# Optimization experiments

Measured on AMD Instinct MI355X. Metric: run time of the kernel, lower is better.

The kernel has to match this reference:

```python
import jax, jax.numpy as jnp
import numpy as np
import math

N_HEADS = 4
IN_DIM = 1024
DIM_HEAD = IN_DIM // N_HEADS


def setup_inputs() -> dict:
    key = jax.random.key(0)
    ks = jax.random.split(key, 5)
    x = jax.random.normal(ks[0], (8, 2048, IN_DIM), dtype=jnp.float32)
    std = 0.02
    W_Q = jax.random.normal(ks[1], (N_HEADS, IN_DIM, DIM_HEAD), dtype=jnp.float32) * std
    W_K = jax.random.normal(ks[2], (N_HEADS, IN_DIM, DIM_HEAD), dtype=jnp.float32) * std
    W_V = jax.random.normal(ks[3], (N_HEADS, IN_DIM, DIM_HEAD), dtype=jnp.float32) * std
    W_O = jax.random.normal(ks[4], (N_HEADS, DIM_HEAD, IN_DIM), dtype=jnp.float32) * std
    b_Q = jnp.zeros((N_HEADS, DIM_HEAD), dtype=jnp.float32)
    b_K = jnp.zeros((N_HEADS, DIM_HEAD), dtype=jnp.float32)
    b_V = jnp.zeros((N_HEADS, DIM_HEAD), dtype=jnp.float32)
    b_O = jnp.zeros((IN_DIM,), dtype=jnp.float32)
    return {"normalized_resid_pre": x, "W_Q": W_Q, "b_Q": b_Q, "W_K": W_K,
            "b_K": b_K, "W_V": W_V, "b_V": b_V, "W_O": W_O, "b_O": b_O}


def reference(normalized_resid_pre, W_Q, b_Q, W_K, b_K, W_V, b_V, W_O, b_O):
    x = normalized_resid_pre  # [n, s, d_model]
    # projections: [n, s, h, dh]
    q = jnp.einsum('nsd,hde->nshe', x, W_Q) + b_Q
    k = jnp.einsum('nsd,hde->nshe', x, W_K) + b_K
    v = jnp.einsum('nsd,hde->nshe', x, W_V) + b_V
    scale = 1.0 / math.sqrt(DIM_HEAD)
    scores = jnp.einsum('nqhe,nkhe->nhqk', q, k) * scale  # [n, h, q, k]
    pattern = jax.nn.softmax(scores, axis=-1)
    z = jnp.einsum('nhqk,nkhe->nqhe', pattern, v)  # [n, q, h, dh]
    out = jnp.einsum('nqhe,hed->nqd', z, W_O) + b_O  # [n, q, d_model]
    return out
```

## Files before the change

kernel.cpp:

```cpp
#include <hip/hip_runtime.h>

typedef __attribute__((ext_vector_type(8))) short short8;
typedef __attribute__((ext_vector_type(4))) float floatx4;
typedef __attribute__((ext_vector_type(16))) float floatx16;
typedef __attribute__((ext_vector_type(4))) unsigned short ushort4v;
typedef __attribute__((ext_vector_type(2))) unsigned int uint2v;
typedef unsigned short u16;

__device__ __forceinline__ u16 f2bf(float f) {
  unsigned u = __float_as_uint(f);
  u += 0x7fffu + ((u >> 16) & 1u);
  return (u16)(u >> 16);
}

__device__ __forceinline__ void gl_lds16(const void* g, void* l) {
  __builtin_amdgcn_global_load_lds((const __attribute__((address_space(1))) void*)g,
                                   (__attribute__((address_space(3))) void*)l, 16, 0, 0);
}

__device__ __forceinline__ float bpermf(float v, int srclane) {
  return __int_as_float(__builtin_amdgcn_ds_bpermute(srclane << 2, __float_as_int(v)));
}

#define BARRIER() do { asm volatile("" ::: "memory"); __builtin_amdgcn_s_barrier(); asm volatile("" ::: "memory"); } while (0)


__global__ void k_cvt_x(const float* __restrict__ x, u16* __restrict__ o, long n) {
  long i = ((long)blockIdx.x * blockDim.x + threadIdx.x) * 8;
  long stride = (long)gridDim.x * blockDim.x * 8;
  for (; i < n; i += stride) {
    float4 a = *(const float4*)(x + i);
    float4 b = *(const float4*)(x + i + 4);
    ushort4v r0 = { f2bf(a.x), f2bf(a.y), f2bf(a.z), f2bf(a.w) };
    ushort4v r1 = { f2bf(b.x), f2bf(b.y), f2bf(b.z), f2bf(b.w) };
    *(ushort4v*)(o + i) = r0;
    *(ushort4v*)(o + i + 4) = r1;
  }
}

__global__ __launch_bounds__(256) void k_cvt_w(
    const float* __restrict__ WQ, const float* __restrict__ WK,
    const float* __restrict__ WV, const float* __restrict__ WO,
    u16* __restrict__ wqkv, u16* __restrict__ wo) {
  __shared__ float tile[64][65];
  const int bid = blockIdx.x;
  const float* src;
  u16* dst;
  int C, R, r0, c0;
  if (bid < 768) {
    int th = bid >> 6;
    int tid6 = bid & 63;
    int t = th >> 2, h = th & 3;
    src = ((t == 0) ? WQ : (t == 1) ? WK : WV) + h * 1024 * 256;
    dst = wqkv + (size_t)(t * 1024 + h * 256) * 1024;
    R = 1024; C = 256;
    r0 = (tid6 & 15) * 64;
    c0 = (tid6 >> 4) * 64;
  } else {
    int tid6 = bid - 768;
    src = WO; dst = wo;
    R = 1024; C = 1024;
    r0 = (tid6 & 15) * 64;
    c0 = (tid6 >> 4) * 64;
  }
  const int tx = threadIdx.x & 15, ty = threadIdx.x >> 4;
#pragma unroll
  for (int i = 0; i < 4; ++i) {
    int r = ty + 16 * i;
    float4 v = *(const float4*)(src + (long)(r0 + r) * C + c0 + tx * 4);
    tile[r][tx * 4 + 0] = v.x;
    tile[r][tx * 4 + 1] = v.y;
    tile[r][tx * 4 + 2] = v.z;
    tile[r][tx * 4 + 3] = v.w;
  }
  __syncthreads();
#pragma unroll
  for (int i = 0; i < 4; ++i) {
    int c = ty + 16 * i;
    ushort4v o = { f2bf(tile[tx * 4 + 0][c]), f2bf(tile[tx * 4 + 1][c]),
                   f2bf(tile[tx * 4 + 2][c]), f2bf(tile[tx * 4 + 3][c]) };
    *(ushort4v*)(dst + (long)(c0 + c) * R + r0 + tx * 4) = o;
  }
}

template<int EPI>
__global__ __launch_bounds__(512, 2) void k_gemm8(
    const u16* __restrict__ A, const u16* __restrict__ Bt,
    u16* __restrict__ Qo, u16* __restrict__ Ko, u16* __restrict__ Vt,
    const float* __restrict__ bQ, const float* __restrict__ bK, const float* __restrict__ bV,
    float* __restrict__ out, const float* __restrict__ bO, int gridNx) {
  extern __shared__ char lds[];
  const int tid = threadIdx.x, lane = tid & 63, w = tid >> 6;
  const int wm = w >> 2, wn = w & 3;
  const int cI = lane & 15, rI = lane >> 4;
  const int nwg = gridDim.x;
  const int bid = blockIdx.x;
  const int swz = (bid & 7) * (nwg >> 3) + (bid >> 3);
  const int by = swz / gridNx, bx = swz % gridNx;
  const long am0 = (long)by * 256, bn0 = (long)bx * 256;

  int so_ds[2], so_src[2];
#pragma unroll
  for (int jj = 0; jj < 2; ++jj) {
    int o = jj * 8192 + tid * 16;
    int row = o >> 7;
    so_ds[jj] = o;
    so_src[jj] = row * 1024 + ((((o >> 4) & 7) ^ (row & 7)) << 3);
  }
  const u16* gAlo = A + am0 * 1024;
  const u16* gAhi = gAlo + 128 * 1024;
  const u16* gBlo = Bt + bn0 * 1024;
  const u16* gBhi = gBlo + 128 * 1024;

#define STG(gp, kt, ldsbyte) do { \
    gl_lds16((gp) + (kt) * 64 + so_src[0], lds + (ldsbyte) + so_ds[0]); \
    gl_lds16((gp) + (kt) * 64 + so_src[1], lds + (ldsbyte) + so_ds[1]); \
  } while (0)

  floatx4 acc[8][4] = {};

  STG(gAlo, 0, 0);
  STG(gBlo, 0, 65536);
  STG(gAhi, 0, 16384);
  STG(gBhi, 0, 81920);
  STG(gAlo, 1, 32768);
  STG(gBlo, 1, 98304);
  asm volatile("s_waitcnt vmcnt(4)" ::: "memory");
  BARRIER();

#define PHASE(AB, BB, MH, NH, STAGE_STMT, VMSTMT) do { \
    short8 af[4][2], bf[2][2]; \
    _Pragma("unroll") \
    for (int mi2 = 0; mi2 < 4; ++mi2) { \
      int row = wm * 64 + mi2 * 16 + cI; \
      const char* rp = lds + (AB) + (MH) * 16384 + row * 128; \
      int sw = row & 7; \
      _Pragma("unroll") \
      for (int kk = 0; kk < 2; ++kk) \
        af[mi2][kk] = *(const short8*)(rp + (((kk * 4 + rI) ^ sw) << 4)); \
    } \
    _Pragma("unroll") \
    for (int ni2 = 0; ni2 < 2; ++ni2) { \
      int row = wn * 32 + ni2 * 16 + cI; \
      const char* rp = lds + (BB) + (NH) * 16384 + row * 128; \
      int sw = row & 7; \
      _Pragma("unroll") \
      for (int kk = 0; kk < 2; ++kk) \
        bf[ni2][kk] = *(const short8*)(rp + (((kk * 4 + rI) ^ sw) << 4)); \
    } \
    STAGE_STMT; \
    VMSTMT; \
    BARRIER(); \
    __builtin_amdgcn_s_setprio(1); \
    _Pragma("unroll") \
    for (int mi2 = 0; mi2 < 4; ++mi2) \
      _Pragma("unroll") \
      for (int ni2 = 0; ni2 < 2; ++ni2) \
        _Pragma("unroll") \
        for (int kk = 0; kk < 2; ++kk) \
          acc[(MH) * 4 + mi2][(NH) * 2 + ni2] = __builtin_amdgcn_mfma_f32_16x16x32_bf16( \
              af[mi2][kk], bf[ni2][kk], acc[(MH) * 4 + mi2][(NH) * 2 + ni2], 0, 0, 0); \
    __builtin_amdgcn_s_setprio(0); \
    BARRIER(); \
  } while (0)

  for (int it = 0; it < 8; ++it) {
    const int u = 2 * it;
    const bool s2 = (u + 2 < 16), s3 = (u + 3 < 16);
    PHASE(0, 65536, 0, 0, STG(gAhi, u + 1, 49152), );
    PHASE(0, 65536, 0, 1, STG(gBhi, u + 1, 114688), );
    PHASE(0, 65536, 1, 0, if (s2) STG(gAlo, u + 2, 0), );
    PHASE(0, 65536, 1, 1, if (s2) STG(gBlo, u + 2, 65536),
          if (s2) { asm volatile("s_waitcnt vmcnt(4)" ::: "memory"); }
          else    { asm volatile("s_waitcnt vmcnt(0)" ::: "memory"); });
    PHASE(32768, 98304, 0, 0, if (s2) STG(gAhi, u + 2, 16384), );
    PHASE(32768, 98304, 0, 1, if (s2) STG(gBhi, u + 2, 81920), );
    PHASE(32768, 98304, 1, 0, if (s3) STG(gAlo, u + 3, 32768), );
    PHASE(32768, 98304, 1, 1, if (s3) STG(gBlo, u + 3, 98304),
          asm volatile("s_waitcnt vmcnt(4)" ::: "memory"));
  }

  if (EPI == 0) {
    const int t = (int)(bn0 >> 10);
    const int h = (int)(bn0 >> 8) & 3;
    const float* bias = (t == 0) ? bQ : (t == 1) ? bK : bV;
    const float sc = (t == 0) ? 0.0625f * 1.44269504088896f : 1.0f;
#pragma unroll
    for (int MH = 0; MH < 2; ++MH)
#pragma unroll
    for (int mi = 0; mi < 4; ++mi) {
      int m = (int)am0 + MH * 128 + wm * 64 + mi * 16 + rI * 4;
      int b = m >> 11, s = m & 2047;
#pragma unroll
      for (int NH = 0; NH < 2; ++NH)
#pragma unroll
      for (int ni = 0; ni < 2; ++ni) {
        int e = NH * 128 + wn * 32 + ni * 16 + cI;
        float bb = bias[h * 256 + e];
        floatx4 c = acc[MH * 4 + mi][NH * 2 + ni];
        if (t == 0) {
          long base = ((long)(b * 4 + h) * 2048 + s) * 256 + e;
          Qo[base]       = f2bf((c[0] + bb) * sc);
          Qo[base + 256] = f2bf((c[1] + bb) * sc);
          Qo[base + 512] = f2bf((c[2] + bb) * sc);
          Qo[base + 768] = f2bf((c[3] + bb) * sc);
        } else if (t == 1) {
          long kb = ((long)(b * 4 + h) << 19) + ((long)(s >> 5) << 13) +
                    ((e >> 3) << 8) + ((s & 31) << 3) + (e & 7);
          Ko[kb]      = f2bf(c[0] + bb);
          Ko[kb + 8]  = f2bf(c[1] + bb);
          Ko[kb + 16] = f2bf(c[2] + bb);
          Ko[kb + 24] = f2bf(c[3] + bb);
        } else {
          long vb = ((long)(b * 4 + h) << 19) + ((long)(s >> 5) << 13) +
                    (((s >> 3) & 3) << 11) + ((long)e << 3) + (s & 7);
          ushort4v v = { f2bf(c[0] + bb), f2bf(c[1] + bb), f2bf(c[2] + bb), f2bf(c[3] + bb) };
          *(ushort4v*)(Vt + vb) = v;
        }
      }
    }
  } else {
#pragma unroll
    for (int MH = 0; MH < 2; ++MH)
#pragma unroll
    for (int mi = 0; mi < 4; ++mi) {
      int m = (int)am0 + MH * 128 + wm * 64 + mi * 16 + rI * 4;
#pragma unroll
      for (int NH = 0; NH < 2; ++NH)
#pragma unroll
      for (int ni = 0; ni < 2; ++ni) {
        int n = (int)bn0 + NH * 128 + wn * 32 + ni * 16 + cI;
        float bb = bO[n];
        floatx4 c = acc[MH * 4 + mi][NH * 2 + ni];
        out[(long)m * 1024 + n]       = c[0] + bb;
        out[(long)(m + 1) * 1024 + n] = c[1] + bb;
        out[(long)(m + 2) * 1024 + n] = c[2] + bb;
        out[(long)(m + 3) * 1024 + n] = c[3] + bb;
      }
    }
  }
#undef PHASE
#undef STG
}

__global__ __launch_bounds__(256, 2) void k_attn(
    const u16* __restrict__ Q, const u16* __restrict__ K,
    const u16* __restrict__ Vt, u16* __restrict__ Z) {
  extern __shared__ u16 smem[];
  char* sKc = (char*)smem;
  char* sVc = (char*)smem + 32768;
  const int tid = threadIdx.x, lane = tid & 63, w = tid >> 6;
  const int q = lane & 31, hi = lane >> 5;
  const int role = (blockIdx.x & 7) * 64 + (blockIdx.x >> 3);
  const int bh = role >> 4, qt = role & 15;
  const long base = (long)bh * 2048 * 256;
  const int q0 = qt * 128 + w * 32;

  const u16* Kg0 = K + base;
  const u16* Vg0 = Vt + base;
  const int stq = tid * 8;
  const int dtq = tid * 16;

  short8 qf[16];
#pragma unroll
  for (int ec = 0; ec < 16; ++ec)
    qf[ec] = *(const short8*)(Q + base + (long)(q0 + q) * 256 + ec * 16 + hi * 8);

#define STAGE_K(kt_, buf_) do { \
    const u16* g_ = Kg0 + (kt_) * 8192 + stq; \
    char* d_ = sKc + (buf_) * 16384 + dtq; \
    _Pragma("unroll") \
    for (int j = 0; j < 4; ++j) gl_lds16(g_ + j * 2048, d_ + j * 4096); \
  } while (0)
#define STAGE_V(kt_, buf_) do { \
    const u16* g_ = Vg0 + (kt_) * 8192 + stq; \
    char* d_ = sVc + (buf_) * 16384 + dtq; \
    _Pragma("unroll") \
    for (int j = 0; j < 4; ++j) gl_lds16(g_ + j * 2048, d_ + j * 4096); \
  } while (0)

  STAGE_K(0, 0);

  floatx16 z[8] = {};
  float m_run = -1e30f, l = 0.f;
  const int kb = hi * 512 + q * 16;
  const int vb = hi * 4096 + q * 16;
  short8 pa0 = {}, pa1 = {};

  __syncthreads();

  for (int t = 0; t < 64; ++t) {
    const int cb = t & 1;
    if (t < 63) STAGE_K(t + 1, cb ^ 1);
    STAGE_V(t, cb);
    const char* pK = sKc + cb * 16384 + kb;
    const char* pV = sVc + (cb ^ 1) * 16384 + vb;

    floatx16 s = {};
    __builtin_amdgcn_s_setprio(1);
    if (t > 0) {
#pragma unroll
      for (int u = 0; u < 8; ++u) {
        short8 kf0 = *(const short8*)(pK + (2 * u) * 1024);
        s = __builtin_amdgcn_mfma_f32_32x32x16_bf16(kf0, qf[2 * u], s, 0, 0, 0);
        short8 vf0 = *(const short8*)(pV + u * 512);
        z[u] = __builtin_amdgcn_mfma_f32_32x32x16_bf16(pa0, vf0, z[u], 0, 0, 0);
        short8 kf1 = *(const short8*)(pK + (2 * u + 1) * 1024);
        s = __builtin_amdgcn_mfma_f32_32x32x16_bf16(kf1, qf[2 * u + 1], s, 0, 0, 0);
        short8 vf1 = *(const short8*)(pV + 8192 + u * 512);
        z[u] = __builtin_amdgcn_mfma_f32_32x32x16_bf16(pa1, vf1, z[u], 0, 0, 0);
      }
    } else {
#pragma unroll
      for (int ec = 0; ec < 16; ++ec) {
        short8 kf = *(const short8*)(pK + ec * 1024);
        s = __builtin_amdgcn_mfma_f32_32x32x16_bf16(kf, qf[ec], s, 0, 0, 0);
      }
    }
    __builtin_amdgcn_s_setprio(0);

    float m0 = fmaxf(s[0], s[1]),  m1 = fmaxf(s[2], s[3]);
    float m2 = fmaxf(s[4], s[5]),  m3 = fmaxf(s[6], s[7]);
    float m4 = fmaxf(s[8], s[9]),  m5 = fmaxf(s[10], s[11]);
    float m6 = fmaxf(s[12], s[13]), m7 = fmaxf(s[14], s[15]);
    m0 = fmaxf(m0, m1); m2 = fmaxf(m2, m3); m4 = fmaxf(m4, m5); m6 = fmaxf(m6, m7);
    m0 = fmaxf(m0, m2); m4 = fmaxf(m4, m6);
    float pm = fmaxf(m0, m4);
    {
      uint2v sw = __builtin_amdgcn_permlane32_swap(__float_as_uint(pm), __float_as_uint(pm), false, false);
      pm = fmaxf(__uint_as_float(sw[0]), __uint_as_float(sw[1]));
    }

    if (!__all(pm <= m_run + 8.f)) {
      float mn = fmaxf(m_run, pm);
      float esc = exp2f(m_run - mn);
      l *= esc;
      m_run = mn;
      float escv[16];
#pragma unroll
      for (int r = 0; r < 16; ++r)
        escv[r] = bpermf(esc, ((r & 3) + 8 * (r >> 2) + 4 * hi) + 32 * hi);
#pragma unroll
      for (int et = 0; et < 8; ++et)
#pragma unroll
        for (int r = 0; r < 16; ++r) z[et][r] *= escv[r];
    }

    float p[16], rs = 0.f;
#pragma unroll
    for (int r = 0; r < 16; ++r) { p[r] = exp2f(s[r] - m_run); rs += p[r]; }
    {
      uint2v sw = __builtin_amdgcn_permlane32_swap(__float_as_uint(rs), __float_as_uint(rs), false, false);
      l += __uint_as_float(sw[0]) + __uint_as_float(sw[1]);
    }

    unsigned w0, w1, w2, w3, w4, w5, w6, w7;
    asm("v_cvt_pk_bf16_f32 %0, %1, %2" : "=v"(w0) : "v"(p[0]), "v"(p[1]));
    asm("v_cvt_pk_bf16_f32 %0, %1, %2" : "=v"(w1) : "v"(p[2]), "v"(p[3]));
    asm("v_cvt_pk_bf16_f32 %0, %1, %2" : "=v"(w2) : "v"(p[4]), "v"(p[5]));
    asm("v_cvt_pk_bf16_f32 %0, %1, %2" : "=v"(w3) : "v"(p[6]), "v"(p[7]));
    asm("v_cvt_pk_bf16_f32 %0, %1, %2" : "=v"(w4) : "v"(p[8]), "v"(p[9]));
    asm("v_cvt_pk_bf16_f32 %0, %1, %2" : "=v"(w5) : "v"(p[10]), "v"(p[11]));
    asm("v_cvt_pk_bf16_f32 %0, %1, %2" : "=v"(w6) : "v"(p[12]), "v"(p[13]));
    asm("v_cvt_pk_bf16_f32 %0, %1, %2" : "=v"(w7) : "v"(p[14]), "v"(p[15]));
    uint2v e02 = __builtin_amdgcn_permlane32_swap(w0, w2, false, false);
    uint2v e13 = __builtin_amdgcn_permlane32_swap(w1, w3, false, false);
    uint2v e46 = __builtin_amdgcn_permlane32_swap(w4, w6, false, false);
    uint2v e57 = __builtin_amdgcn_permlane32_swap(w5, w7, false, false);
    int4 t0i = { (int)e02[0], (int)e13[0], (int)e02[1], (int)e13[1] };
    int4 t1i = { (int)e46[0], (int)e57[0], (int)e46[1], (int)e57[1] };
    pa0 = *(short8*)&t0i;
    pa1 = *(short8*)&t1i;

    __syncthreads();
  }

  {
    const char* pV = sVc + 16384 + vb;
#pragma unroll
    for (int u = 0; u < 8; ++u) {
      short8 vf0 = *(const short8*)(pV + u * 512);
      z[u] = __builtin_amdgcn_mfma_f32_32x32x16_bf16(pa0, vf0, z[u], 0, 0, 0);
      short8 vf1 = *(const short8*)(pV + 8192 + u * 512);
      z[u] = __builtin_amdgcn_mfma_f32_32x32x16_bf16(pa1, vf1, z[u], 0, 0, 0);
    }
  }

  float linv = 1.f / l;
  float invv[16];
#pragma unroll
  for (int r = 0; r < 16; ++r)
    invv[r] = bpermf(linv, ((r & 3) + 8 * (r >> 2) + 4 * hi) + 32 * hi);

  const int b = bh >> 2, hh = bh & 3;
  const long zb = (long)b * 2048 * 1024 + hh * 256;
#pragma unroll
  for (int r = 0; r < 16; ++r) {
    const int qr = (r & 3) + 8 * (r >> 2) + 4 * hi;
    long rb = zb + (long)(q0 + qr) * 1024;
#pragma unroll
    for (int et = 0; et < 8; ++et)
      Z[rb + et * 32 + q] = f2bf(z[et][r] * invv[r]);
  }
#undef STAGE_K
#undef STAGE_V
}


extern "C" void kernel_launch(void* const* d_in, const int* in_sizes, int n_in,
                              void* d_out, int out_size, void* d_ws, size_t ws_size,
                              hipStream_t stream) {
  const float* x  = (const float*)d_in[0];
  const float* WQ = (const float*)d_in[1];
  const float* bQ = (const float*)d_in[2];
  const float* WK = (const float*)d_in[3];
  const float* bK = (const float*)d_in[4];
  const float* WV = (const float*)d_in[5];
  const float* bV = (const float*)d_in[6];
  const float* WO = (const float*)d_in[7];
  const float* bO = (const float*)d_in[8];
  float* out = (float*)d_out;

  char* p = (char*)d_ws;
  u16* xb   = (u16*)p; p += (size_t)16384 * 1024 * 2;
  u16* wqkv = (u16*)p; p += (size_t)3072 * 1024 * 2;
  u16* wo   = (u16*)p; p += (size_t)1024 * 1024 * 2;
  u16* Qb   = (u16*)p; p += (size_t)32 * 2048 * 256 * 2;
  u16* Kb   = (u16*)p; p += (size_t)32 * 2048 * 256 * 2;
  u16* Vtb  = (u16*)p; p += (size_t)32 * 256 * 2048 * 2;
  u16* Zb   = xb;

  const int attn_lds = 65536;
  (void)hipFuncSetAttribute((const void*)k_attn,
                            hipFuncAttributeMaxDynamicSharedMemorySize, attn_lds);
  const int gemm_lds = 131072;
  (void)hipFuncSetAttribute((const void*)k_gemm8<0>,
                            hipFuncAttributeMaxDynamicSharedMemorySize, gemm_lds);
  (void)hipFuncSetAttribute((const void*)k_gemm8<1>,
                            hipFuncAttributeMaxDynamicSharedMemorySize, gemm_lds);

  k_cvt_x<<<dim3(4096), dim3(256), 0, stream>>>(x, xb, (long)16384 * 1024);
  k_cvt_w<<<dim3(1024), dim3(256), 0, stream>>>(WQ, WK, WV, WO, wqkv, wo);
  k_gemm8<0><<<dim3(768), dim3(512), gemm_lds, stream>>>(xb, wqkv, Qb, Kb, Vtb, bQ, bK, bV,
                                                         (float*)nullptr, (const float*)nullptr, 12);
  k_attn<<<dim3(512), dim3(256), attn_lds, stream>>>(Qb, Kb, Vtb, Zb);
  k_gemm8<1><<<dim3(256), dim3(512), gemm_lds, stream>>>(Zb, wo,
                                                         (u16*)nullptr, (u16*)nullptr, (u16*)nullptr,
                                                         (const float*)nullptr, (const float*)nullptr, (const float*)nullptr,
                                                         out, bO, 4);
}
```

Measured before the change: 325.3 us.

## Double attention query tile per block and remap GEMM/attention blocks per XCD

The attention kernel now runs 512 threads per block covering 256 query rows, so each staged K/V tile in LDS serves eight waves instead of four. The staging loops are halved to match, giving half the global-to-LDS traffic per query row. The QK^T MFMA chain is split into two independent accumulators, and the softmax row sum becomes a tree reduction, to shorten dependency chains. Both GEMM launches and the attention launch also get an explicit XCD-aware block-to-tile mapping meant to improve L2 locality. The cost is fewer, larger blocks (one per CU), which may cause tail imbalance, and extra vector adds to merge the split accumulators.

```diff
diff --git a/kernel.cpp b/kernel.cpp
--- a/kernel.cpp
+++ b/kernel.cpp
@@ -93,10 +93,11 @@
   const int tid = threadIdx.x, lane = tid & 63, w = tid >> 6;
   const int wm = w >> 2, wn = w & 3;
   const int cI = lane & 15, rI = lane >> 4;
-  const int nwg = gridDim.x;
   const int bid = blockIdx.x;
-  const int swz = (bid & 7) * (nwg >> 3) + (bid >> 3);
-  const int by = swz / gridNx, bx = swz % gridNx;
+  const int xcd = bid & 7, ii = bid >> 3;
+  const int by = xcd * 8 + (ii & 7);
+  const int bx = ii >> 3;
+  (void)gridNx;
   const long am0 = (long)by * 256, bn0 = (long)bx * 256;
 
   int so_ds[2], so_src[2];
@@ -243,7 +244,7 @@
 #undef STG
 }
 
-__global__ __launch_bounds__(256, 2) void k_attn(
+__global__ __launch_bounds__(512, 1) void k_attn(
     const u16* __restrict__ Q, const u16* __restrict__ K,
     const u16* __restrict__ Vt, u16* __restrict__ Z) {
   extern __shared__ u16 smem[];
@@ -251,10 +252,11 @@
   char* sVc = (char*)smem + 32768;
   const int tid = threadIdx.x, lane = tid & 63, w = tid >> 6;
   const int q = lane & 31, hi = lane >> 5;
-  const int role = (blockIdx.x & 7) * 64 + (blockIdx.x >> 3);
-  const int bh = role >> 4, qt = role & 15;
+  const int xcd = blockIdx.x & 7, bi = blockIdx.x >> 3;
+  const int bh = xcd * 4 + (bi & 3);
+  const int qt = bi >> 2;
   const long base = (long)bh * 2048 * 256;
-  const int q0 = qt * 128 + w * 32;
+  const int q0 = qt * 256 + w * 32;
 
   const u16* Kg0 = K + base;
   const u16* Vg0 = Vt + base;
@@ -269,14 +271,14 @@
 #define STAGE_K(kt_, buf_) do { \
     const u16* g_ = Kg0 + (kt_) * 8192 + stq; \
     char* d_ = sKc + (buf_) * 16384 + dtq; \
-    _Pragma("unroll") \
-    for (int j = 0; j < 4; ++j) gl_lds16(g_ + j * 2048, d_ + j * 4096); \
+    gl_lds16(g_, d_); \
+    gl_lds16(g_ + 4096, d_ + 8192); \
   } while (0)
 #define STAGE_V(kt_, buf_) do { \
     const u16* g_ = Vg0 + (kt_) * 8192 + stq; \
     char* d_ = sVc + (buf_) * 16384 + dtq; \
-    _Pragma("unroll") \
-    for (int j = 0; j < 4; ++j) gl_lds16(g_ + j * 2048, d_ + j * 4096); \
+    gl_lds16(g_, d_); \
+    gl_lds16(g_ + 4096, d_ + 8192); \
   } while (0)
 
   STAGE_K(0, 0);
@@ -296,28 +298,31 @@
     const char* pK = sKc + cb * 16384 + kb;
     const char* pV = sVc + (cb ^ 1) * 16384 + vb;
 
-    floatx16 s = {};
+    floatx16 s0 = {}, s1 = {};
     __builtin_amdgcn_s_setprio(1);
     if (t > 0) {
 #pragma unroll
       for (int u = 0; u < 8; ++u) {
         short8 kf0 = *(const short8*)(pK + (2 * u) * 1024);
-        s = __builtin_amdgcn_mfma_f32_32x32x16_bf16(kf0, qf[2 * u], s, 0, 0, 0);
+        s0 = __builtin_amdgcn_mfma_f32_32x32x16_bf16(kf0, qf[2 * u], s0, 0, 0, 0);
         short8 vf0 = *(const short8*)(pV + u * 512);
         z[u] = __builtin_amdgcn_mfma_f32_32x32x16_bf16(pa0, vf0, z[u], 0, 0, 0);
         short8 kf1 = *(const short8*)(pK + (2 * u + 1) * 1024);
-        s = __builtin_amdgcn_mfma_f32_32x32x16_bf16(kf1, qf[2 * u + 1], s, 0, 0, 0);
+        s1 = __builtin_amdgcn_mfma_f32_32x32x16_bf16(kf1, qf[2 * u + 1], s1, 0, 0, 0);
         short8 vf1 = *(const short8*)(pV + 8192 + u * 512);
         z[u] = __builtin_amdgcn_mfma_f32_32x32x16_bf16(pa1, vf1, z[u], 0, 0, 0);
       }
     } else {
 #pragma unroll
-      for (int ec = 0; ec < 16; ++ec) {
-        short8 kf = *(const short8*)(pK + ec * 1024);
-        s = __builtin_amdgcn_mfma_f32_32x32x16_bf16(kf, qf[ec], s, 0, 0, 0);
+      for (int u = 0; u < 8; ++u) {
+        short8 kf0 = *(const short8*)(pK + (2 * u) * 1024);
+        s0 = __builtin_amdgcn_mfma_f32_32x32x16_bf16(kf0, qf[2 * u], s0, 0, 0, 0);
+        short8 kf1 = *(const short8*)(pK + (2 * u + 1) * 1024);
+        s1 = __builtin_amdgcn_mfma_f32_32x32x16_bf16(kf1, qf[2 * u + 1], s1, 0, 0, 0);
       }
     }
     __builtin_amdgcn_s_setprio(0);
+    floatx16 s = s0 + s1;
 
     float m0 = fmaxf(s[0], s[1]),  m1 = fmaxf(s[2], s[3]);
     float m2 = fmaxf(s[4], s[5]),  m3 = fmaxf(s[6], s[7]);
@@ -346,9 +351,14 @@
         for (int r = 0; r < 16; ++r) z[et][r] *= escv[r];
     }
 
-    float p[16], rs = 0.f;
-#pragma unroll
-    for (int r = 0; r < 16; ++r) { p[r] = exp2f(s[r] - m_run); rs += p[r]; }
+    float p[16];
+#pragma unroll
+    for (int r = 0; r < 16; ++r) p[r] = exp2f(s[r] - m_run);
+    float a0 = p[0] + p[1], a1 = p[2] + p[3], a2 = p[4] + p[5], a3 = p[6] + p[7];
+    float a4 = p[8] + p[9], a5 = p[10] + p[11], a6 = p[12] + p[13], a7 = p[14] + p[15];
+    a0 += a1; a2 += a3; a4 += a5; a6 += a7;
+    a0 += a2; a4 += a6;
+    float rs = a0 + a4;
     {
       uint2v sw = __builtin_amdgcn_permlane32_swap(__float_as_uint(rs), __float_as_uint(rs), false, false);
       l += __uint_as_float(sw[0]) + __uint_as_float(sw[1]);
@@ -443,7 +453,7 @@
   k_cvt_w<<<dim3(1024), dim3(256), 0, stream>>>(WQ, WK, WV, WO, wqkv, wo);
   k_gemm8<0><<<dim3(768), dim3(512), gemm_lds, stream>>>(xb, wqkv, Qb, Kb, Vtb, bQ, bK, bV,
                                                          (float*)nullptr, (const float*)nullptr, 12);
-  k_attn<<<dim3(512), dim3(256), attn_lds, stream>>>(Qb, Kb, Vtb, Zb);
+  k_attn<<<dim3(256), dim3(512), attn_lds, stream>>>(Qb, Kb, Vtb, Zb);
   k_gemm8<1><<<dim3(256), dim3(512), gemm_lds, stream>>>(Zb, wo,
                                                          (u16*)nullptr, (u16*)nullptr, (u16*)nullptr,
                                                          (const float*)nullptr, (const float*)nullptr, (const float*)nullptr,
```

Measured after the change: 324.6 us. Within noise of the previous version (-0.2%).
